# Kernel optimization log

Measured on AMD Instinct MI355X. Metric: run time of the kernel, lower is better.

## Reference

```python
import jax, jax.numpy as jnp
import numpy as np

B, N, D = 4, 1024, 1024   # batch, seq (x and context must match), model dim
H, DH = 16, 64            # heads, dim_head; inner_dim = H*DH = 1024
INNER = H * DH
EPS = 1e-5


def setup_inputs() -> dict:
    key = jax.random.key(0)
    ks = jax.random.split(key, 12)
    s = 0.02
    return {
        "x": jax.random.normal(ks[0], (B, N, D), dtype=jnp.float32),
        "context": jax.random.normal(ks[1], (B, N, D), dtype=jnp.float32),
        # weights stored as [in, out] (torch Linear weight transposed)
        "W_qk": jax.random.normal(ks[2], (D, INNER), dtype=jnp.float32) * s,
        "W_cqk": jax.random.normal(ks[3], (D, INNER), dtype=jnp.float32) * s,
        "W_v": jax.random.normal(ks[4], (D, INNER), dtype=jnp.float32) * s,
        "W_cv": jax.random.normal(ks[5], (D, INNER), dtype=jnp.float32) * s,
        "W_out": jax.random.normal(ks[6], (INNER, D), dtype=jnp.float32) * s,
        "b_out": jax.random.normal(ks[7], (D,), dtype=jnp.float32) * s,
        "W_cout": jax.random.normal(ks[8], (INNER, D), dtype=jnp.float32) * s,
        "b_cout": jax.random.normal(ks[9], (D,), dtype=jnp.float32) * s,
        "gamma": jnp.ones((D,), dtype=jnp.float32),
        "beta": jnp.zeros((D,), dtype=jnp.float32),
    }


def _split_heads(t):  # [b, n, h*d] -> [b, h, n, d]
    b, n, _ = t.shape
    return t.reshape(b, n, H, DH).transpose(0, 2, 1, 3)


def _merge_heads(t):  # [b, h, n, d] -> [b, n, h*d]
    b, h, n, d = t.shape
    return t.transpose(0, 2, 1, 3).reshape(b, n, h * d)


def _layernorm(y, gamma, beta):
    mu = jnp.mean(y, axis=-1, keepdims=True)
    var = jnp.var(y, axis=-1, keepdims=True)
    return gamma * (y - mu) * jax.lax.rsqrt(var + EPS) + beta


def reference(x, context, W_qk, W_cqk, W_v, W_cv, W_out, b_out, W_cout, b_cout, gamma, beta):
    scale = DH ** -0.5
    res = x + context                       # residual (requires identical shapes)
    # prenorm=False -> identity norms; dropout=0; talking_heads=False -> identity
    qk = _split_heads(x @ W_qk)             # [b,h,i,d]
    v = _split_heads(x @ W_v)               # [b,h,i,d]
    cqk = _split_heads(context @ W_cqk)     # [b,h,j,d]
    cv = _split_heads(context @ W_cv)       # [b,h,j,d]

    sim = jnp.einsum('bhid,bhjd->bhij', qk, cqk) * scale  # shared similarity
    attn = jax.nn.softmax(sim, axis=-1)      # row softmax (x attends to context)
    context_attn = jax.nn.softmax(sim, axis=-2)  # column softmax (context attends to x)

    out = jnp.einsum('bhij,bhjd->bhid', attn, cv)          # [b,h,i,d]
    context_out = jnp.einsum('bhji,bhjd->bhid', context_attn, v)  # [b,h,i,d]

    out = _merge_heads(out) @ W_out + b_out
    context_out = _merge_heads(context_out) @ W_cout + b_cout
    return _layernorm(out + context_out, gamma, beta) + res
```

## Files before the change

kernel.cpp:

```cpp
#include <hip/hip_runtime.h>
#include <hip/hip_bf16.h>

typedef unsigned short u16;
typedef __bf16 bf16x8 __attribute__((ext_vector_type(8)));
typedef float   f32x4 __attribute__((ext_vector_type(4)));
typedef u16     u16x8 __attribute__((ext_vector_type(8)));
typedef u16     u16x4 __attribute__((ext_vector_type(4)));

#define DEV static __device__ __forceinline__

DEV float bf2f(u16 b) { unsigned int u = ((unsigned int)b) << 16; return __builtin_bit_cast(float, u); }
DEV u16   f2bf(float f) { return __builtin_bit_cast(u16, (__bf16)f); }
DEV bf16x8 ldb(const u16* p) { return __builtin_bit_cast(bf16x8, *(const u16x8*)p); }

DEV f32x4 mfma_bf16(bf16x8 a, bf16x8 b, f32x4 c) {
  return __builtin_amdgcn_mfma_f32_16x16x32_bf16(a, b, c, 0, 0, 0);
}

#define LDA 40

__global__ __launch_bounds__(256) void detect_dtype(const u16* x, int* flag) {
  int tid = threadIdx.x;
  u16 lo = x[tid * 2];
  float v = bf2f(lo);
  float av = fabsf(v);
  bool plaus = (av > 1e-4f && av < 50.f);
  __shared__ int cnt;
  if (tid == 0) cnt = 0;
  __syncthreads();
  if (plaus) atomicAdd(&cnt, 1);
  __syncthreads();
  if (tid == 0) *flag = (cnt >= 128) ? 1 : 0;
}

struct Cv2 { const void* s[2]; u16* d[2]; };
__global__ __launch_bounds__(256) void convert_big(Cv2 p, const int* flagp) {
  int fl = *flagp;
  const void* src = p.s[blockIdx.z];
  u16* dst = p.d[blockIdx.z];
  size_t i = ((size_t)blockIdx.x * 256 + threadIdx.x) * 8;
  if (fl) {
    *(u16x8*)(dst + i) = *(const u16x8*)((const u16*)src + i);
  } else {
    const float* s = (const float*)src + i;
    u16x8 o;
#pragma unroll
    for (int k = 0; k < 8; ++k) o[k] = f2bf(s[k]);
    *(u16x8*)(dst + i) = o;
  }
}

struct Sm4 { const void* s[4]; u16* d[4]; };
__global__ __launch_bounds__(256) void convert_smalls(Sm4 p, const int* flagp) {
  int fl = *flagp;
  const void* src = p.s[blockIdx.x];
  u16* dst = p.d[blockIdx.x];
  int i = threadIdx.x * 4;
#pragma unroll
  for (int k = 0; k < 4; ++k)
    dst[i + k] = fl ? ((const u16*)src)[i + k] : f2bf(((const float*)src)[i + k]);
}

struct T6 { const void* s[6]; u16* d[6]; };

__global__ __launch_bounds__(256) void transpose6(T6 t, const int* flagp) {
  int fl = *flagp;
  __shared__ u16 tile[32][33];
  const void* src = t.s[blockIdx.z];
  u16* dst = t.d[blockIdx.z];
  int x0 = blockIdx.x * 32, y0 = blockIdx.y * 32;
  int tx = threadIdx.x & 31, ty = threadIdx.x >> 5;
#pragma unroll
  for (int i = 0; i < 32; i += 8) {
    size_t idx = (size_t)(y0 + ty + i) * 1024 + x0 + tx;
    tile[ty + i][tx] = fl ? ((const u16*)src)[idx] : f2bf(((const float*)src)[idx]);
  }
  __syncthreads();
#pragma unroll
  for (int i = 0; i < 32; i += 8)
    dst[(size_t)(x0 + ty + i) * 1024 + y0 + tx] = tile[tx][ty + i];
}

struct Proj4 { const u16* A[4]; const u16* Bt[4]; u16* C[4]; int mode[4]; };

__global__ __launch_bounds__(256) void gemm_proj(Proj4 p) {
  const int K = 1024, Nn = 1024;
  const u16* A  = p.A[blockIdx.z];
  const u16* Bt = p.Bt[blockIdx.z];
  u16* C = p.C[blockIdx.z];
  int mode = p.mode[blockIdx.z];

  __shared__ __align__(16) u16 As[128 * LDA];
  __shared__ __align__(16) u16 Bs[128 * LDA];

  int tid = threadIdx.x, lane = tid & 63, w = tid >> 6;
  int wm = w & 1, wn = w >> 1;
  int q4 = lane >> 4, c = lane & 15;
  int m0 = blockIdx.y * 128, n0 = blockIdx.x * 128;

  int ar = 32 * w + (lane >> 2);
  int ag = (lane & 3) * 8;
  int sa = ar * LDA + ag;

  const u16* pA = A  + (size_t)(m0 + ar) * K + ag;
  const u16* pB = Bt + (size_t)(n0 + ar) * K + ag;

  u16x8 a0 = *(const u16x8*)(pA);
  u16x8 a1 = *(const u16x8*)(pA + (size_t)16 * K);
  u16x8 b0 = *(const u16x8*)(pB);
  u16x8 b1 = *(const u16x8*)(pB + (size_t)16 * K);

  f32x4 acc[4][4] = {};

  for (int k0 = 0; k0 < K; k0 += 32) {
    __syncthreads();
    *(u16x8*)(As + sa)            = a0;
    *(u16x8*)(As + sa + 16 * LDA) = a1;
    *(u16x8*)(Bs + sa)            = b0;
    *(u16x8*)(Bs + sa + 16 * LDA) = b1;
    __syncthreads();
    if (k0 + 32 < K) {
      a0 = *(const u16x8*)(pA + k0 + 32);
      a1 = *(const u16x8*)(pA + (size_t)16 * K + k0 + 32);
      b0 = *(const u16x8*)(pB + k0 + 32);
      b1 = *(const u16x8*)(pB + (size_t)16 * K + k0 + 32);
    }
    bf16x8 af[4], bfr[4];
#pragma unroll
    for (int i = 0; i < 4; ++i) af[i]  = ldb(As + (wm * 64 + i * 16 + c) * LDA + q4 * 8);
#pragma unroll
    for (int j = 0; j < 4; ++j) bfr[j] = ldb(Bs + (wn * 64 + j * 16 + c) * LDA + q4 * 8);
#pragma unroll
    for (int i = 0; i < 4; ++i)
#pragma unroll
      for (int j = 0; j < 4; ++j)
        acc[i][j] = mfma_bf16(af[i], bfr[j], acc[i][j]);
  }

  if (mode == 0) {
#pragma unroll
    for (int i = 0; i < 4; ++i) {
      int mrow = m0 + wm * 64 + i * 16 + q4 * 4;
#pragma unroll
      for (int j = 0; j < 4; ++j) {
        int col = n0 + wn * 64 + j * 16 + c;
#pragma unroll
        for (int r = 0; r < 4; ++r)
          C[(size_t)(mrow + r) * Nn + col] = f2bf(acc[i][j][r]);
      }
    }
  } else {
    int bidx = m0 >> 10;
#pragma unroll
    for (int i = 0; i < 4; ++i) {
      int mrow = m0 + wm * 64 + i * 16 + q4 * 4;
      int jj = mrow & 1023;
#pragma unroll
      for (int j = 0; j < 4; ++j) {
        int col = n0 + wn * 64 + j * 16 + c;
        int h = col >> 6, dh = col & 63;
        u16x4 pk;
#pragma unroll
        for (int r = 0; r < 4; ++r) pk[r] = f2bf(acc[i][j][r]);
        *(u16x4*)(C + ((size_t)((bidx * 16 + h) * 64 + dh)) * 1024 + jj) = pk;
      }
    }
  }
}

__global__ __launch_bounds__(256) void flash_attn(const u16* Q, const u16* Kg,
                                                  const u16* Vt, u16* O) {
  int bh = blockIdx.y; int b = bh >> 4, h = bh & 15;
  int i0 = blockIdx.x * 64;
  int tid = threadIdx.x, lane = tid & 63, w = tid >> 6;
  int q4 = lane >> 4, c = lane & 15;

  __shared__ __align__(16) u16 Ks[64 * 72];
  __shared__ __align__(16) u16 Vs[64 * 72];
  __shared__ __align__(16) u16 Ps[4][16 * 72];

  const size_t qoff = ((size_t)(b * 1024 + i0 + w * 16 + c)) * 1024 + h * 64 + q4 * 8;
  bf16x8 qf0 = ldb(Q + qoff);
  bf16x8 qf1 = ldb(Q + qoff + 32);

  f32x4 of[4] = {};
  f32x4 lacc = {};
  bf16x8 ones;
#pragma unroll
  for (int k = 0; k < 8; ++k) ones[k] = (__bf16)1.0f;

  int jr = tid >> 2, seg = (tid & 3) * 16;
  const u16* krow_base = Kg + ((size_t)(b * 1024 + jr)) * 1024 + h * 64 + seg;
  const u16* vrow_base = Vt + ((size_t)((b * 16 + h) * 64 + jr)) * 1024 + seg;
  const float scale = 0.125f;

  for (int j0 = 0; j0 < 1024; j0 += 64) {
    const u16* ks = krow_base + (size_t)j0 * 1024;
    u16x8 kv0 = *(const u16x8*)(ks);
    u16x8 kv1 = *(const u16x8*)(ks + 8);
    const u16* vs = vrow_base + j0;
    u16x8 vv0 = *(const u16x8*)(vs);
    u16x8 vv1 = *(const u16x8*)(vs + 8);
    __syncthreads();
    *(u16x8*)(Ks + jr * 72 + seg)     = kv0;
    *(u16x8*)(Ks + jr * 72 + seg + 8) = kv1;
    *(u16x8*)(Vs + jr * 72 + seg)     = vv0;
    *(u16x8*)(Vs + jr * 72 + seg + 8) = vv1;
    __syncthreads();

    f32x4 sf[4] = {};
#pragma unroll
    for (int jc = 0; jc < 4; ++jc) {
      bf16x8 k0f = ldb(Ks + (jc * 16 + c) * 72 + q4 * 8);
      bf16x8 k1f = ldb(Ks + (jc * 16 + c) * 72 + 32 + q4 * 8);
      sf[jc] = mfma_bf16(k0f, qf0, sf[jc]);
      sf[jc] = mfma_bf16(k1f, qf1, sf[jc]);
    }

#pragma unroll
    for (int jc = 0; jc < 4; ++jc) {
      u16x4 pk;
#pragma unroll
      for (int r = 0; r < 4; ++r) {
        float s = fminf(fmaxf(sf[jc][r] * scale, -60.f), 60.f);
        pk[r] = f2bf(__expf(s));
      }
      *(u16x4*)(Ps[w] + c * 72 + jc * 16 + q4 * 4) = pk;
    }

    asm volatile("s_waitcnt lgkmcnt(0)" ::: "memory");

    bf16x8 pf0 = ldb(Ps[w] + c * 72 + q4 * 8);
    bf16x8 pf1 = ldb(Ps[w] + c * 72 + 32 + q4 * 8);

    lacc = mfma_bf16(pf0, ones, lacc);
    lacc = mfma_bf16(pf1, ones, lacc);

#pragma unroll
    for (int dc = 0; dc < 4; ++dc) {
      bf16x8 v0f = ldb(Vs + (dc * 16 + c) * 72 + q4 * 8);
      bf16x8 v1f = ldb(Vs + (dc * 16 + c) * 72 + 32 + q4 * 8);
      of[dc] = mfma_bf16(pf0, v0f, of[dc]);
      of[dc] = mfma_bf16(pf1, v1f, of[dc]);
    }
  }

  float inv[4];
#pragma unroll
  for (int r = 0; r < 4; ++r) inv[r] = 1.0f / lacc[r];
#pragma unroll
  for (int dc = 0; dc < 4; ++dc) {
    int col = h * 64 + dc * 16 + c;
#pragma unroll
    for (int r = 0; r < 4; ++r) {
      int irow = i0 + w * 16 + q4 * 4 + r;
      O[((size_t)(b * 1024 + irow)) * 1024 + col] = f2bf(of[dc][r] * inv[r]);
    }
  }
}

__global__ __launch_bounds__(256) void gemm_final(const u16* A1, const u16* B1t,
                                                  const u16* A2, const u16* B2t,
                                                  const u16* b1, const u16* b2,
                                                  float* Y) {
  const int K = 1024, Nn = 1024;
  __shared__ __align__(16) u16 As[128 * LDA];
  __shared__ __align__(16) u16 Bs[128 * LDA];

  int tid = threadIdx.x, lane = tid & 63, w = tid >> 6;
  int wm = w & 1, wn = w >> 1;
  int q4 = lane >> 4, c = lane & 15;
  int m0 = blockIdx.y * 128, n0 = blockIdx.x * 128;

  int ar = 32 * w + (lane >> 2);
  int ag = (lane & 3) * 8;
  int sa = ar * LDA + ag;

  const u16* A1b = A1 + (size_t)(m0 + ar) * K + ag;
  const u16* A2b = A2 + (size_t)(m0 + ar) * K + ag;
  const u16* B1b = B1t + (size_t)(n0 + ar) * K + ag;
  const u16* B2b = B2t + (size_t)(n0 + ar) * K + ag;

  u16x8 a0 = *(const u16x8*)(A1b);
  u16x8 a1 = *(const u16x8*)(A1b + (size_t)16 * K);
  u16x8 b0 = *(const u16x8*)(B1b);
  u16x8 b1v = *(const u16x8*)(B1b + (size_t)16 * K);

  f32x4 acc[4][4] = {};

  for (int kk = 0; kk < 64; ++kk) {
    __syncthreads();
    *(u16x8*)(As + sa)            = a0;
    *(u16x8*)(As + sa + 16 * LDA) = a1;
    *(u16x8*)(Bs + sa)            = b0;
    *(u16x8*)(Bs + sa + 16 * LDA) = b1v;
    __syncthreads();
    if (kk + 1 < 64) {
      const u16* An = (kk + 1 < 32) ? A1b : A2b;
      const u16* Bn = (kk + 1 < 32) ? B1b : B2b;
      int k0n = ((kk + 1) & 31) * 32;
      a0  = *(const u16x8*)(An + k0n);
      a1  = *(const u16x8*)(An + (size_t)16 * K + k0n);
      b0  = *(const u16x8*)(Bn + k0n);
      b1v = *(const u16x8*)(Bn + (size_t)16 * K + k0n);
    }
    bf16x8 af[4], bfr[4];
#pragma unroll
    for (int i = 0; i < 4; ++i) af[i]  = ldb(As + (wm * 64 + i * 16 + c) * LDA + q4 * 8);
#pragma unroll
    for (int j = 0; j < 4; ++j) bfr[j] = ldb(Bs + (wn * 64 + j * 16 + c) * LDA + q4 * 8);
#pragma unroll
    for (int i = 0; i < 4; ++i)
#pragma unroll
      for (int j = 0; j < 4; ++j)
        acc[i][j] = mfma_bf16(af[i], bfr[j], acc[i][j]);
  }

#pragma unroll
  for (int i = 0; i < 4; ++i) {
    int mrow = m0 + wm * 64 + i * 16 + q4 * 4;
#pragma unroll
    for (int j = 0; j < 4; ++j) {
      int col = n0 + wn * 64 + j * 16 + c;
      float bias = bf2f(b1[col]) + bf2f(b2[col]);
#pragma unroll
      for (int r = 0; r < 4; ++r)
        Y[(size_t)(mrow + r) * Nn + col] = acc[i][j][r] + bias;
    }
  }
}

__global__ __launch_bounds__(256) void ln_res(const float* Y, const u16* gamma, const u16* beta,
                                              const u16* x, const u16* ctx, void* out,
                                              const int* flagp) {
  int fl = *flagp;
  int row = blockIdx.x;
  int tid = threadIdx.x;
  const float* y = Y + (size_t)row * 1024;
  float4 v = *(const float4*)(y + tid * 4);
  float s  = v.x + v.y + v.z + v.w;
  float s2 = v.x * v.x + v.y * v.y + v.z * v.z + v.w * v.w;
#pragma unroll
  for (int off = 1; off < 64; off <<= 1) { s += __shfl_xor(s, off); s2 += __shfl_xor(s2, off); }
  __shared__ float red[8];
  int w = tid >> 6, lane = tid & 63;
  if (lane == 0) { red[w] = s; red[w + 4] = s2; }
  __syncthreads();
  float S  = red[0] + red[1] + red[2] + red[3];
  float S2 = red[4] + red[5] + red[6] + red[7];
  float mu  = S * (1.0f / 1024.0f);
  float var = S2 * (1.0f / 1024.0f) - mu * mu;
  float rs = rsqrtf(var + 1e-5f);
  size_t base = (size_t)row * 1024 + tid * 4;
  u16x4 gv = *(const u16x4*)(gamma + tid * 4);
  u16x4 bv = *(const u16x4*)(beta + tid * 4);
  u16x4 xv = *(const u16x4*)(x + base);
  u16x4 cv = *(const u16x4*)(ctx + base);
  float vv[4] = {v.x, v.y, v.z, v.w};
  float o[4];
#pragma unroll
  for (int k = 0; k < 4; ++k)
    o[k] = bf2f(gv[k]) * (vv[k] - mu) * rs + bf2f(bv[k]) + bf2f(xv[k]) + bf2f(cv[k]);
  if (fl) {
    u16x4 ov;
#pragma unroll
    for (int k = 0; k < 4; ++k) ov[k] = f2bf(o[k]);
    *(u16x4*)((u16*)out + base) = ov;
  } else {
    *(float4*)((float*)out + base) = make_float4(o[0], o[1], o[2], o[3]);
  }
}

__global__ __launch_bounds__(256) void sentinel(u16* out) {
  size_t i = ((size_t)blockIdx.x * 256 + threadIdx.x) * 8;
  u16 v = f2bf(12345.0f);
  u16x8 o = {v, v, v, v, v, v, v, v};
  *(u16x8*)(out + i) = o;
}

extern "C" void kernel_launch(void* const* d_in, const int* in_sizes, int n_in,
                              void* d_out, int out_size, void* d_ws, size_t ws_size,
                              hipStream_t stream) {
  (void)in_sizes; (void)n_in; (void)out_size;
  const size_t MB = 1024 * 1024;
  const size_t NEED = 61 * MB;
  if (ws_size < NEED) {
    sentinel<<<2048, 256, 0, stream>>>((u16*)d_out);
    return;
  }

  char* ws = (char*)d_ws;
  u16* wt[6];
  for (int i = 0; i < 6; ++i) wt[i] = (u16*)(ws + (size_t)i * 2 * MB);
  u16* xc   = (u16*)(ws + 12 * MB);
  u16* cc   = (u16*)(ws + 20 * MB);
  u16* qk   = (u16*)(ws + 28 * MB);
  u16* cqk  = (u16*)(ws + 36 * MB);
  u16* vt   = (u16*)(ws + 44 * MB);
  u16* cvt  = (u16*)(ws + 52 * MB);
  u16* oa   = (u16*)(ws + 0);
  u16* ca   = (u16*)(ws + 52 * MB);
  float* y  = (float*)(ws + 28 * MB);
  int* flag = (int*)(ws + 60 * MB);
  u16* b1c  = (u16*)(ws + 60 * MB + 4096);
  u16* b2c  = (u16*)(ws + 60 * MB + 8192);
  u16* gc   = (u16*)(ws + 60 * MB + 12288);
  u16* bc   = (u16*)(ws + 60 * MB + 16384);

  detect_dtype<<<1, 256, 0, stream>>>((const u16*)d_in[0], flag);

  Cv2 cv;
  cv.s[0] = d_in[0]; cv.d[0] = xc;
  cv.s[1] = d_in[1]; cv.d[1] = cc;
  convert_big<<<dim3(2048, 1, 2), 256, 0, stream>>>(cv, flag);

  Sm4 sm;
  sm.s[0] = d_in[7]; sm.d[0] = b1c;
  sm.s[1] = d_in[9]; sm.d[1] = b2c;
  sm.s[2] = d_in[10]; sm.d[2] = gc;
  sm.s[3] = d_in[11]; sm.d[3] = bc;
  convert_smalls<<<4, 256, 0, stream>>>(sm, flag);

  T6 t;
  t.s[0] = d_in[2]; t.d[0] = wt[0];
  t.s[1] = d_in[3]; t.d[1] = wt[1];
  t.s[2] = d_in[4]; t.d[2] = wt[2];
  t.s[3] = d_in[5]; t.d[3] = wt[3];
  t.s[4] = d_in[6]; t.d[4] = wt[4];
  t.s[5] = d_in[8]; t.d[5] = wt[5];
  transpose6<<<dim3(32, 32, 6), 256, 0, stream>>>(t, flag);

  Proj4 p;
  p.A[0] = xc; p.Bt[0] = wt[0]; p.C[0] = qk;  p.mode[0] = 0;
  p.A[1] = cc; p.Bt[1] = wt[1]; p.C[1] = cqk; p.mode[1] = 0;
  p.A[2] = xc; p.Bt[2] = wt[2]; p.C[2] = vt;  p.mode[2] = 1;
  p.A[3] = cc; p.Bt[3] = wt[3]; p.C[3] = cvt; p.mode[3] = 1;
  gemm_proj<<<dim3(8, 32, 4), 256, 0, stream>>>(p);

  flash_attn<<<dim3(16, 64), 256, 0, stream>>>(qk, cqk, cvt, oa);
  flash_attn<<<dim3(16, 64), 256, 0, stream>>>(cqk, qk, vt, ca);

  gemm_final<<<dim3(8, 32), 256, 0, stream>>>(oa, wt[4], ca, wt[5], b1c, b2c, y);

  ln_res<<<4096, 256, 0, stream>>>(y, gc, bc, xc, cc, d_out, flag);
}
```

Before: 295.6 us.

## Batch attention launches, double query rows per block, double-buffer final GEMM

The two flash-attention launches become one launch indexed by blockIdx.z, and each block now processes 128 query rows instead of 64, so every K/V tile loaded into shared memory is reused twice. The final GEMM gains double-buffered shared memory with a single barrier per k-step. Shared-memory row padding is removed (stride 40 becomes 32) in both GEMMs. Unpadded rows can cause LDS bank conflicts, halving the attention grid lowers block count and occupancy, and the double buffer doubles shared-memory use.

```diff
diff --git a/kernel.cpp b/kernel.cpp
--- a/kernel.cpp
+++ b/kernel.cpp
@@ -17,7 +17,7 @@
   return __builtin_amdgcn_mfma_f32_16x16x32_bf16(a, b, c, 0, 0, 0);
 }
 
-#define LDA 40
+#define LDK 32
 
 __global__ __launch_bounds__(256) void detect_dtype(const u16* x, int* flag) {
   int tid = threadIdx.x;
@@ -90,8 +90,8 @@
   u16* C = p.C[blockIdx.z];
   int mode = p.mode[blockIdx.z];
 
-  __shared__ __align__(16) u16 As[128 * LDA];
-  __shared__ __align__(16) u16 Bs[128 * LDA];
+  __shared__ __align__(16) u16 As[128 * LDK];
+  __shared__ __align__(16) u16 Bs[128 * LDK];
 
   int tid = threadIdx.x, lane = tid & 63, w = tid >> 6;
   int wm = w & 1, wn = w >> 1;
@@ -100,7 +100,7 @@
 
   int ar = 32 * w + (lane >> 2);
   int ag = (lane & 3) * 8;
-  int sa = ar * LDA + ag;
+  int sa = ar * LDK + ag;
 
   const u16* pA = A  + (size_t)(m0 + ar) * K + ag;
   const u16* pB = Bt + (size_t)(n0 + ar) * K + ag;
@@ -115,9 +115,9 @@
   for (int k0 = 0; k0 < K; k0 += 32) {
     __syncthreads();
     *(u16x8*)(As + sa)            = a0;
-    *(u16x8*)(As + sa + 16 * LDA) = a1;
+    *(u16x8*)(As + sa + 16 * LDK) = a1;
     *(u16x8*)(Bs + sa)            = b0;
-    *(u16x8*)(Bs + sa + 16 * LDA) = b1;
+    *(u16x8*)(Bs + sa + 16 * LDK) = b1;
     __syncthreads();
     if (k0 + 32 < K) {
       a0 = *(const u16x8*)(pA + k0 + 32);
@@ -127,9 +127,9 @@
     }
     bf16x8 af[4], bfr[4];
 #pragma unroll
-    for (int i = 0; i < 4; ++i) af[i]  = ldb(As + (wm * 64 + i * 16 + c) * LDA + q4 * 8);
-#pragma unroll
-    for (int j = 0; j < 4; ++j) bfr[j] = ldb(Bs + (wn * 64 + j * 16 + c) * LDA + q4 * 8);
+    for (int i = 0; i < 4; ++i) af[i]  = ldb(As + (wm * 64 + i * 16 + c) * LDK + q4 * 8);
+#pragma unroll
+    for (int j = 0; j < 4; ++j) bfr[j] = ldb(Bs + (wn * 64 + j * 16 + c) * LDK + q4 * 8);
 #pragma unroll
     for (int i = 0; i < 4; ++i)
 #pragma unroll
@@ -168,23 +168,33 @@
   }
 }
 
-__global__ __launch_bounds__(256) void flash_attn(const u16* Q, const u16* Kg,
-                                                  const u16* Vt, u16* O) {
+struct FA { const u16* Q[2]; const u16* K[2]; const u16* V[2]; u16* O[2]; };
+
+__global__ __launch_bounds__(256) void flash_attn(FA fa) {
+  const u16* Q  = fa.Q[blockIdx.z];
+  const u16* Kg = fa.K[blockIdx.z];
+  const u16* Vt = fa.V[blockIdx.z];
+  u16* O        = fa.O[blockIdx.z];
+
   int bh = blockIdx.y; int b = bh >> 4, h = bh & 15;
-  int i0 = blockIdx.x * 64;
+  int i0 = blockIdx.x * 128;
   int tid = threadIdx.x, lane = tid & 63, w = tid >> 6;
   int q4 = lane >> 4, c = lane & 15;
 
   __shared__ __align__(16) u16 Ks[64 * 72];
   __shared__ __align__(16) u16 Vs[64 * 72];
-  __shared__ __align__(16) u16 Ps[4][16 * 72];
-
-  const size_t qoff = ((size_t)(b * 1024 + i0 + w * 16 + c)) * 1024 + h * 64 + q4 * 8;
-  bf16x8 qf0 = ldb(Q + qoff);
-  bf16x8 qf1 = ldb(Q + qoff + 32);
-
-  f32x4 of[4] = {};
-  f32x4 lacc = {};
+  __shared__ __align__(16) u16 Ps[4][32 * 72];
+
+  bf16x8 qf[2][2];
+#pragma unroll
+  for (int hf = 0; hf < 2; ++hf) {
+    const size_t qoff = ((size_t)(b * 1024 + i0 + hf * 64 + w * 16 + c)) * 1024 + h * 64 + q4 * 8;
+    qf[hf][0] = ldb(Q + qoff);
+    qf[hf][1] = ldb(Q + qoff + 32);
+  }
+
+  f32x4 of[2][4] = {};
+  f32x4 lacc[2] = {};
   bf16x8 ones;
 #pragma unroll
   for (int k = 0; k < 8; ++k) ones[k] = (__bf16)1.0f;
@@ -208,53 +218,67 @@
     *(u16x8*)(Vs + jr * 72 + seg + 8) = vv1;
     __syncthreads();
 
-    f32x4 sf[4] = {};
+    f32x4 sf[2][4] = {};
 #pragma unroll
     for (int jc = 0; jc < 4; ++jc) {
       bf16x8 k0f = ldb(Ks + (jc * 16 + c) * 72 + q4 * 8);
       bf16x8 k1f = ldb(Ks + (jc * 16 + c) * 72 + 32 + q4 * 8);
-      sf[jc] = mfma_bf16(k0f, qf0, sf[jc]);
-      sf[jc] = mfma_bf16(k1f, qf1, sf[jc]);
-    }
-
-#pragma unroll
-    for (int jc = 0; jc < 4; ++jc) {
-      u16x4 pk;
-#pragma unroll
-      for (int r = 0; r < 4; ++r) {
-        float s = fminf(fmaxf(sf[jc][r] * scale, -60.f), 60.f);
-        pk[r] = f2bf(__expf(s));
-      }
-      *(u16x4*)(Ps[w] + c * 72 + jc * 16 + q4 * 4) = pk;
-    }
+#pragma unroll
+      for (int hf = 0; hf < 2; ++hf) {
+        sf[hf][jc] = mfma_bf16(k0f, qf[hf][0], sf[hf][jc]);
+        sf[hf][jc] = mfma_bf16(k1f, qf[hf][1], sf[hf][jc]);
+      }
+    }
+
+#pragma unroll
+    for (int hf = 0; hf < 2; ++hf)
+#pragma unroll
+      for (int jc = 0; jc < 4; ++jc) {
+        u16x4 pk;
+#pragma unroll
+        for (int r = 0; r < 4; ++r) {
+          float s = fminf(fmaxf(sf[hf][jc][r] * scale, -60.f), 60.f);
+          pk[r] = f2bf(__expf(s));
+        }
+        *(u16x4*)(Ps[w] + (hf * 16 + c) * 72 + jc * 16 + q4 * 4) = pk;
+      }
 
     asm volatile("s_waitcnt lgkmcnt(0)" ::: "memory");
 
-    bf16x8 pf0 = ldb(Ps[w] + c * 72 + q4 * 8);
-    bf16x8 pf1 = ldb(Ps[w] + c * 72 + 32 + q4 * 8);
-
-    lacc = mfma_bf16(pf0, ones, lacc);
-    lacc = mfma_bf16(pf1, ones, lacc);
+    bf16x8 pf[2][2];
+#pragma unroll
+    for (int hf = 0; hf < 2; ++hf) {
+      pf[hf][0] = ldb(Ps[w] + (hf * 16 + c) * 72 + q4 * 8);
+      pf[hf][1] = ldb(Ps[w] + (hf * 16 + c) * 72 + 32 + q4 * 8);
+      lacc[hf] = mfma_bf16(pf[hf][0], ones, lacc[hf]);
+      lacc[hf] = mfma_bf16(pf[hf][1], ones, lacc[hf]);
+    }
 
 #pragma unroll
     for (int dc = 0; dc < 4; ++dc) {
       bf16x8 v0f = ldb(Vs + (dc * 16 + c) * 72 + q4 * 8);
       bf16x8 v1f = ldb(Vs + (dc * 16 + c) * 72 + 32 + q4 * 8);
-      of[dc] = mfma_bf16(pf0, v0f, of[dc]);
-      of[dc] = mfma_bf16(pf1, v1f, of[dc]);
-    }
-  }
-
-  float inv[4];
-#pragma unroll
-  for (int r = 0; r < 4; ++r) inv[r] = 1.0f / lacc[r];
-#pragma unroll
-  for (int dc = 0; dc < 4; ++dc) {
-    int col = h * 64 + dc * 16 + c;
-#pragma unroll
-    for (int r = 0; r < 4; ++r) {
-      int irow = i0 + w * 16 + q4 * 4 + r;
-      O[((size_t)(b * 1024 + irow)) * 1024 + col] = f2bf(of[dc][r] * inv[r]);
+#pragma unroll
+      for (int hf = 0; hf < 2; ++hf) {
+        of[hf][dc] = mfma_bf16(pf[hf][0], v0f, of[hf][dc]);
+        of[hf][dc] = mfma_bf16(pf[hf][1], v1f, of[hf][dc]);
+      }
+    }
+  }
+
+#pragma unroll
+  for (int hf = 0; hf < 2; ++hf) {
+    float inv[4];
+#pragma unroll
+    for (int r = 0; r < 4; ++r) inv[r] = 1.0f / lacc[hf][r];
+#pragma unroll
+    for (int dc = 0; dc < 4; ++dc) {
+      int col = h * 64 + dc * 16 + c;
+#pragma unroll
+      for (int r = 0; r < 4; ++r) {
+        int irow = i0 + hf * 64 + w * 16 + q4 * 4 + r;
+        O[((size_t)(b * 1024 + irow)) * 1024 + col] = f2bf(of[hf][dc][r] * inv[r]);
+      }
     }
   }
 }
@@ -264,8 +288,8 @@
                                                   const u16* b1, const u16* b2,
                                                   float* Y) {
   const int K = 1024, Nn = 1024;
-  __shared__ __align__(16) u16 As[128 * LDA];
-  __shared__ __align__(16) u16 Bs[128 * LDA];
+  __shared__ __align__(16) u16 As[2][128 * LDK];
+  __shared__ __align__(16) u16 Bs[2][128 * LDK];
 
   int tid = threadIdx.x, lane = tid & 63, w = tid >> 6;
   int wm = w & 1, wn = w >> 1;
@@ -274,7 +298,7 @@
 
   int ar = 32 * w + (lane >> 2);
   int ag = (lane & 3) * 8;
-  int sa = ar * LDA + ag;
+  int sa = ar * LDK + ag;
 
   const u16* A1b = A1 + (size_t)(m0 + ar) * K + ag;
   const u16* A2b = A2 + (size_t)(m0 + ar) * K + ag;
@@ -286,15 +310,16 @@
   u16x8 b0 = *(const u16x8*)(B1b);
   u16x8 b1v = *(const u16x8*)(B1b + (size_t)16 * K);
 
+  *(u16x8*)(As[0] + sa)            = a0;
+  *(u16x8*)(As[0] + sa + 16 * LDK) = a1;
+  *(u16x8*)(Bs[0] + sa)            = b0;
+  *(u16x8*)(Bs[0] + sa + 16 * LDK) = b1v;
+  __syncthreads();
+
   f32x4 acc[4][4] = {};
 
   for (int kk = 0; kk < 64; ++kk) {
-    __syncthreads();
-    *(u16x8*)(As + sa)            = a0;
-    *(u16x8*)(As + sa + 16 * LDA) = a1;
-    *(u16x8*)(Bs + sa)            = b0;
-    *(u16x8*)(Bs + sa + 16 * LDA) = b1v;
-    __syncthreads();
+    int p = kk & 1;
     if (kk + 1 < 64) {
       const u16* An = (kk + 1 < 32) ? A1b : A2b;
       const u16* Bn = (kk + 1 < 32) ? B1b : B2b;
@@ -303,17 +328,22 @@
       a1  = *(const u16x8*)(An + (size_t)16 * K + k0n);
       b0  = *(const u16x8*)(Bn + k0n);
       b1v = *(const u16x8*)(Bn + (size_t)16 * K + k0n);
+      *(u16x8*)(As[1 - p] + sa)            = a0;
+      *(u16x8*)(As[1 - p] + sa + 16 * LDK) = a1;
+      *(u16x8*)(Bs[1 - p] + sa)            = b0;
+      *(u16x8*)(Bs[1 - p] + sa + 16 * LDK) = b1v;
     }
     bf16x8 af[4], bfr[4];
 #pragma unroll
-    for (int i = 0; i < 4; ++i) af[i]  = ldb(As + (wm * 64 + i * 16 + c) * LDA + q4 * 8);
-#pragma unroll
-    for (int j = 0; j < 4; ++j) bfr[j] = ldb(Bs + (wn * 64 + j * 16 + c) * LDA + q4 * 8);
+    for (int i = 0; i < 4; ++i) af[i]  = ldb(As[p] + (wm * 64 + i * 16 + c) * LDK + q4 * 8);
+#pragma unroll
+    for (int j = 0; j < 4; ++j) bfr[j] = ldb(Bs[p] + (wn * 64 + j * 16 + c) * LDK + q4 * 8);
 #pragma unroll
     for (int i = 0; i < 4; ++i)
 #pragma unroll
       for (int j = 0; j < 4; ++j)
         acc[i][j] = mfma_bf16(af[i], bfr[j], acc[i][j]);
+    __syncthreads();
   }
 
 #pragma unroll
@@ -437,8 +467,10 @@
   p.A[3] = cc; p.Bt[3] = wt[3]; p.C[3] = cvt; p.mode[3] = 1;
   gemm_proj<<<dim3(8, 32, 4), 256, 0, stream>>>(p);
 
-  flash_attn<<<dim3(16, 64), 256, 0, stream>>>(qk, cqk, cvt, oa);
-  flash_attn<<<dim3(16, 64), 256, 0, stream>>>(cqk, qk, vt, ca);
+  FA fa;
+  fa.Q[0] = qk;  fa.K[0] = cqk; fa.V[0] = cvt; fa.O[0] = oa;
+  fa.Q[1] = cqk; fa.K[1] = qk;  fa.V[1] = vt;  fa.O[1] = ca;
+  flash_attn<<<dim3(8, 64, 2), 256, 0, stream>>>(fa);
 
   gemm_final<<<dim3(8, 32), 256, 0, stream>>>(oa, wt[4], ca, wt[5], b1c, b2c, y);
 
```

Measured after the change: 298.2 us. Within noise of the previous version (+0.9%).
